# Performance work log

Hardware: AMD Instinct MI355X
Metric: run time of the kernel (lower is better)

## Reference

```python
import jax, jax.numpy as jnp
import numpy as np

KERNEL = 7
STRIDE = 1
DILATION = 1


def _unfold(x, k, d, pad, stride):
    """torch.nn.Unfold semantics on NCHW input -> [n, c, k*k, oh*ow]."""
    n, c, H, W = x.shape
    eff = d * (k - 1) + 1
    oh = (H + 2 * pad - eff) // stride + 1
    ow = (W + 2 * pad - eff) // stride + 1
    xp = jnp.pad(x, ((0, 0), (0, 0), (pad, pad), (pad, pad)))
    # k*k static slices of the padded map, each strided to the output grid
    cols = [
        xp[:, :, i * d : i * d + (oh - 1) * stride + 1 : stride,
              j * d : j * d + (ow - 1) * stride + 1 : stride]
        for i in range(k) for j in range(k)
    ]
    return jnp.stack(cols, axis=2).reshape(n, c, k * k, oh * ow)


def setup_inputs() -> dict:
    key = jax.random.key(0)
    k1, k2 = jax.random.split(key)
    input1 = jax.random.normal(k1, (8, 32, 112, 112), dtype=jnp.float32)
    input2 = jax.random.normal(k2, (8, 32, 112, 112), dtype=jnp.float32)
    return {"input1": input1, "input2": input2}


def reference(input1, input2):
    n, c, H, W = input1.shape
    pad = (DILATION * (KERNEL - 1) + 1) // 2  # module derives its own zero padding
    eff = DILATION * (KERNEL - 1) + 1
    oh = (H + 2 * pad - eff) // STRIDE + 1
    ow = (W + 2 * pad - eff) // STRIDE + 1
    # unfold_i: kernel=1, padding=0 -> strided center samples, shape [n,c,1,L]
    ui = _unfold(input1, 1, DILATION, 0, STRIDE)  # [n, c, 1, H'*W']
    uj = _unfold(input2, KERNEL, DILATION, pad, STRIDE)  # [n, c, k*k, oh*ow]
    # broadcast subtraction: center feature minus each of the k^2 neighbors
    return ui.reshape(n, c, 1, oh * ow) - uj
```

## Files before the change

### kernel.cpp

```cpp
#include <hip/hip_runtime.h>


#define HW     112
#define PLANE  12544
#define KK     49
#define NC_TOT 256
#define YB     16
#define LROWS  22
#define LDSW   132

typedef float f4 __attribute__((ext_vector_type(4)));

__global__ __launch_bounds__(448) void sub2_kernel(
    const float* __restrict__ in1,
    const float* __restrict__ in2,
    float* __restrict__ out)
{
    __shared__ float smem[LROWS * LDSW];

    const int b   = blockIdx.x;
    const int nc  = b / 7;
    const int yb  = b - nc * 7;
    const int y0  = yb * YB;
    const int tid = threadIdx.x;

    {
        const f4 z = {0.f, 0.f, 0.f, 0.f};
        for (int idx = tid; idx < (LROWS * LDSW) / 4; idx += 448)
            reinterpret_cast<f4*>(smem)[idx] = z;
    }
    __syncthreads();

    const float* b_pl = in2 + (size_t)nc * PLANE;
    for (int idx = tid; idx < LROWS * 28; idx += 448) {
        const int r  = idx / 28;
        const int c  = idx - r * 28;
        const int gy = y0 - 3 + r;
        if (gy >= 0 && gy < HW) {
            *reinterpret_cast<f4*>(&smem[r * LDSW + 8 + 4 * c]) =
                *reinterpret_cast<const f4*>(b_pl + gy * HW + 4 * c);
        }
    }
    __syncthreads();

    const int yl = tid / 28;
    const int x0 = (tid - yl * 28) * 4;
    const int y  = y0 + yl;

    const f4 a = *reinterpret_cast<const f4*>(
        in1 + (size_t)nc * PLANE + y * HW + x0);
    float* o_base = out + (size_t)nc * KK * PLANE + (size_t)y * HW + x0;

    #pragma unroll
    for (int i = 0; i < 7; ++i) {
        const float* wr = &smem[(yl + i) * LDSW + 4 + x0];
        const f4 w0 = *reinterpret_cast<const f4*>(wr);
        const f4 w1 = *reinterpret_cast<const f4*>(wr + 4);
        const f4 w2 = *reinterpret_cast<const f4*>(wr + 8);
        const f4 w3 = *reinterpret_cast<const f4*>(wr + 12);
        float wf[16];
        wf[0]=w0.x;  wf[1]=w0.y;  wf[2]=w0.z;  wf[3]=w0.w;
        wf[4]=w1.x;  wf[5]=w1.y;  wf[6]=w1.z;  wf[7]=w1.w;
        wf[8]=w2.x;  wf[9]=w2.y;  wf[10]=w2.z; wf[11]=w2.w;
        wf[12]=w3.x; wf[13]=w3.y; wf[14]=w3.z; wf[15]=w3.w;

        #pragma unroll
        for (int j = 0; j < 7; ++j) {
            f4 r;
            r.x = a.x - wf[j + 1];
            r.y = a.y - wf[j + 2];
            r.z = a.z - wf[j + 3];
            r.w = a.w - wf[j + 4];
            *reinterpret_cast<f4*>(o_base + (size_t)(i * 7 + j) * PLANE) = r;
        }
    }
}

extern "C" void kernel_launch(void* const* d_in, const int* in_sizes, int n_in,
                              void* d_out, int out_size, void* d_ws, size_t ws_size,
                              hipStream_t stream) {
    const float* in1 = (const float*)d_in[0];
    const float* in2 = (const float*)d_in[1];
    float* out = (float*)d_out;

    const int blocks = NC_TOT * 7;
    sub2_kernel<<<blocks, 448, 0, stream>>>(in1, in2, out);
}
```

Measured before the change: 128.6 us.

## Process a whole channel plane per block with a shared zero row for padding

Each block now stages an entire 112x112 plane of input2 in LDS, with a 120-float pitch and one extra zero row used for out-of-range vertical taps. It then writes all 49 output planes for that channel using 1024 threads that each handle up to four positions. This removes the halo rows that were reloaded by every 16-row tile and cuts the launch to 256 blocks. The cost is about 54KB of LDS per block and only 256 blocks on a GPU with many CUs, which lowers occupancy and may leave CUs idle or unevenly loaded on a store-bandwidth-bound kernel.

```diff
diff --git a/kernel.cpp b/kernel.cpp
--- a/kernel.cpp
+++ b/kernel.cpp
@@ -5,65 +5,31 @@
 #define PLANE  12544
 #define KK     49
 #define NC_TOT 256
-#define YB     16
-#define LROWS  22
-#define LDSW   132
+#define PITCH  120
+#define ZROW   112
+#define LDS_F  ((HW + 1) * PITCH)
 
 typedef float f4 __attribute__((ext_vector_type(4)));
 
-__global__ __launch_bounds__(448) void sub2_kernel(
-    const float* __restrict__ in1,
-    const float* __restrict__ in2,
-    float* __restrict__ out)
+__device__ __forceinline__ void process_pos(
+    const float* __restrict__ s2, float* __restrict__ o_nc, int e, f4 a)
 {
-    __shared__ float smem[LROWS * LDSW];
-
-    const int b   = blockIdx.x;
-    const int nc  = b / 7;
-    const int yb  = b - nc * 7;
-    const int y0  = yb * YB;
-    const int tid = threadIdx.x;
-
-    {
-        const f4 z = {0.f, 0.f, 0.f, 0.f};
-        for (int idx = tid; idx < (LROWS * LDSW) / 4; idx += 448)
-            reinterpret_cast<f4*>(smem)[idx] = z;
-    }
-    __syncthreads();
-
-    const float* b_pl = in2 + (size_t)nc * PLANE;
-    for (int idx = tid; idx < LROWS * 28; idx += 448) {
-        const int r  = idx / 28;
-        const int c  = idx - r * 28;
-        const int gy = y0 - 3 + r;
-        if (gy >= 0 && gy < HW) {
-            *reinterpret_cast<f4*>(&smem[r * LDSW + 8 + 4 * c]) =
-                *reinterpret_cast<const f4*>(b_pl + gy * HW + 4 * c);
-        }
-    }
-    __syncthreads();
-
-    const int yl = tid / 28;
-    const int x0 = (tid - yl * 28) * 4;
-    const int y  = y0 + yl;
-
-    const f4 a = *reinterpret_cast<const f4*>(
-        in1 + (size_t)nc * PLANE + y * HW + x0);
-    float* o_base = out + (size_t)nc * KK * PLANE + (size_t)y * HW + x0;
+    const int y  = (4 * e) / HW;
+    const int x0 = 4 * e - y * HW;
+    float* o = o_nc + 4 * e;
 
     #pragma unroll
     for (int i = 0; i < 7; ++i) {
-        const float* wr = &smem[(yl + i) * LDSW + 4 + x0];
+        const int iy  = y + i - 3;
+        const int row = (iy >= 0 && iy < HW) ? iy : ZROW;
+        const float* wr = s2 + row * PITCH + x0;
         const f4 w0 = *reinterpret_cast<const f4*>(wr);
         const f4 w1 = *reinterpret_cast<const f4*>(wr + 4);
         const f4 w2 = *reinterpret_cast<const f4*>(wr + 8);
-        const f4 w3 = *reinterpret_cast<const f4*>(wr + 12);
-        float wf[16];
-        wf[0]=w0.x;  wf[1]=w0.y;  wf[2]=w0.z;  wf[3]=w0.w;
-        wf[4]=w1.x;  wf[5]=w1.y;  wf[6]=w1.z;  wf[7]=w1.w;
-        wf[8]=w2.x;  wf[9]=w2.y;  wf[10]=w2.z; wf[11]=w2.w;
-        wf[12]=w3.x; wf[13]=w3.y; wf[14]=w3.z; wf[15]=w3.w;
-
+        float wf[12];
+        wf[0]=w0.x; wf[1]=w0.y; wf[2] =w0.z; wf[3] =w0.w;
+        wf[4]=w1.x; wf[5]=w1.y; wf[6] =w1.z; wf[7] =w1.w;
+        wf[8]=w2.x; wf[9]=w2.y; wf[10]=w2.z; wf[11]=w2.w;
         #pragma unroll
         for (int j = 0; j < 7; ++j) {
             f4 r;
@@ -71,9 +37,56 @@
             r.y = a.y - wf[j + 2];
             r.z = a.z - wf[j + 3];
             r.w = a.w - wf[j + 4];
-            *reinterpret_cast<f4*>(o_base + (size_t)(i * 7 + j) * PLANE) = r;
+            *reinterpret_cast<f4*>(o + (size_t)(i * 7 + j) * PLANE) = r;
         }
     }
+}
+
+__global__ __launch_bounds__(1024) void sub2_kernel(
+    const float* __restrict__ in1,
+    const float* __restrict__ in2,
+    float* __restrict__ out)
+{
+    __shared__ float s2[LDS_F];
+
+    const int nc = blockIdx.x;
+    const int t  = threadIdx.x;
+
+    const float* a_pl = in1 + (size_t)nc * PLANE;
+    const float* b_pl = in2 + (size_t)nc * PLANE;
+    float*       o_nc = out + (size_t)nc * KK * PLANE;
+
+    const f4 a0 = *reinterpret_cast<const f4*>(a_pl + 4 * t);
+    const f4 a1 = *reinterpret_cast<const f4*>(a_pl + 4 * (t + 1024));
+    const f4 a2 = *reinterpret_cast<const f4*>(a_pl + 4 * (t + 2048));
+    f4 a3 = {0.f, 0.f, 0.f, 0.f};
+    if (t < 64) a3 = *reinterpret_cast<const f4*>(a_pl + 4 * (t + 3072));
+
+    {
+        const f4 z = {0.f, 0.f, 0.f, 0.f};
+        #pragma unroll
+        for (int k = 0; k < 4; ++k) {
+            const int s = t + 1024 * k;
+            if (s < LDS_F / 4) reinterpret_cast<f4*>(s2)[s] = z;
+        }
+    }
+    __syncthreads();
+    #pragma unroll
+    for (int k = 0; k < 4; ++k) {
+        const int s = t + 1024 * k;
+        if (s < 28 * HW) {
+            const int r = s / 28;
+            const int c = s - r * 28;
+            *reinterpret_cast<f4*>(&s2[r * PITCH + 4 + 4 * c]) =
+                *reinterpret_cast<const f4*>(b_pl + r * HW + 4 * c);
+        }
+    }
+    __syncthreads();
+
+    process_pos(s2, o_nc, t, a0);
+    process_pos(s2, o_nc, t + 1024, a1);
+    process_pos(s2, o_nc, t + 2048, a2);
+    if (t < 64) process_pos(s2, o_nc, t + 3072, a3);
 }
 
 extern "C" void kernel_launch(void* const* d_in, const int* in_sizes, int n_in,
@@ -83,6 +96,5 @@
     const float* in2 = (const float*)d_in[1];
     float* out = (float*)d_out;
 
-    const int blocks = NC_TOT * 7;
-    sub2_kernel<<<blocks, 448, 0, stream>>>(in1, in2, out);
+    sub2_kernel<<<NC_TOT, 1024, 0, stream>>>(in1, in2, out);
 }
```

Result: no change. 129.6 us (+0.8%).
